# Kernel optimization log

Hardware: AMD Instinct MI355X
Metric: run time of the kernel (lower is better)

The kernel has to match this reference:

```python
import jax, jax.numpy as jnp
import numpy as np

N = 100_000      # nodes
E = 1_600_000    # edges
F_IN = 512       # input node features
H = 128          # hidden (num_hidden)
C = 64           # num_classes


def setup_inputs() -> dict:
    key = jax.random.key(0)
    ks = jax.random.split(key, 16)
    def lin(k, fi, fo):
        return (jax.random.normal(k, (fi, fo), jnp.float32) / np.sqrt(fi)).astype(jnp.float32)
    inp = {
        'x': jax.random.normal(ks[0], (N, F_IN), jnp.float32),
        'edge_index': jax.random.randint(ks[1], (2, E), 0, N, jnp.int32),
        'W0': lin(ks[2], F_IN, H), 'b0': jnp.zeros((H,), jnp.float32),
        'W1': lin(ks[3], H, H),    'b1': jnp.zeros((H,), jnp.float32),
        'W2': lin(ks[4], H, H),    'b2': jnp.zeros((H,), jnp.float32),
        'fc1_w': lin(ks[5], H, H), 'fc1_b': jnp.zeros((H,), jnp.float32),
        'fc2_w': lin(ks[6], H, H), 'fc2_b': jnp.zeros((H,), jnp.float32),
        'fc3_w': lin(ks[7], H, C), 'fc3_b': jnp.zeros((C,), jnp.float32),
    }
    return inp


def _gcn_norm(edge_index):
    # PyG GCNConv: add self-loops, symmetric normalization deg^-1/2 A deg^-1/2
    src = jnp.concatenate([edge_index[0], jnp.arange(N, dtype=edge_index.dtype)])
    dst = jnp.concatenate([edge_index[1], jnp.arange(N, dtype=edge_index.dtype)])
    deg = jax.ops.segment_sum(jnp.ones_like(dst, jnp.float32), dst, num_segments=N)
    dinv = jnp.where(deg > 0, jax.lax.rsqrt(deg), 0.0)
    norm = dinv[src] * dinv[dst]  # [E+N]
    return src, dst, norm


def _gcn_conv(x, W, b, src, dst, norm):
    h = x @ W + b                      # [N, H] transform first (fewer flops when F_in > H)
    msg = h[src] * norm[:, None]       # gather + scale, [E+N, H]
    return jax.ops.segment_sum(msg, dst, num_segments=N)  # scatter-add


def reference(x, edge_index, W0, b0, W1, b1, W2, b2,
              fc1_w, fc1_b, fc2_w, fc2_b, fc3_w, fc3_b):
    src, dst, norm = _gcn_norm(edge_index)
    y = jax.nn.relu(_gcn_conv(x, W0, b0, src, dst, norm))
    y = jax.nn.relu(_gcn_conv(y, W1, b1, src, dst, norm))
    y = jax.nn.relu(_gcn_conv(y, W2, b2, src, dst, norm))
    y = jax.nn.relu(y @ fc1_w + fc1_b)
    y = jax.nn.relu(y @ fc2_w + fc2_b)
    y = y @ fc3_w + fc3_b
    return jax.nn.log_softmax(y, axis=1)
```

## Files before the change

kernel.cpp:

```cpp
#include <hip/hip_runtime.h>
#include <hip/hip_bf16.h>
#include <cstdint>

typedef __hip_bfloat16 bf16;
typedef __hip_bfloat162 bf162;
typedef __bf16 bf16x8 __attribute__((ext_vector_type(8)));
typedef float f32x4 __attribute__((ext_vector_type(4)));

__global__ void detect_kernel(const unsigned short* __restrict__ xr, int* __restrict__ flag) {
  if (threadIdx.x == 0 && blockIdx.x == 0) {
    int pass = 0;
    for (int i = 0; i < 64; ++i) {
      unsigned short h = xr[2 * i];
      int e = (h >> 7) & 0xFF;
      if (e >= 110 && e <= 140) pass++;
    }
    *flag = (pass >= 32) ? 1 : 0;
  }
}

struct CvtDesc {
  const void* src;
  void* dst;
  int n, fi, fo, mode;
};
struct CvtAll { CvtDesc d[12]; };

__global__ void convert_all_kernel(CvtAll all, const int* __restrict__ flag) {
  CvtDesc dd = all.d[blockIdx.y];
  int isbf = *flag;
  for (int i = blockIdx.x * blockDim.x + threadIdx.x; i < dd.n; i += gridDim.x * blockDim.x) {
    float v = isbf ? __bfloat162float(((const bf16*)dd.src)[i]) : ((const float*)dd.src)[i];
    if (dd.mode) {
      int k = i / dd.fo, nn = i - k * dd.fo;
      ((__bf16*)dd.dst)[(size_t)nn * dd.fi + k] = (__bf16)v;
    } else {
      ((float*)dd.dst)[i] = v;
    }
  }
}


__global__ void count_kernel(const int* __restrict__ dst, int* __restrict__ deg, int E) {
  int i = blockIdx.x * blockDim.x + threadIdx.x;
  if (i < E) atomicAdd(&deg[dst[i]], 1);
}

__global__ void dinv_kernel(const int* __restrict__ deg, float* __restrict__ dinv, int n) {
  int i = blockIdx.x * blockDim.x + threadIdx.x;
  if (i < n) dinv[i] = rsqrtf((float)(deg[i] + 1));
}

__global__ void scan_block_kernel(const int* __restrict__ counts, int* __restrict__ excl,
                                  int* __restrict__ bsum, int n) {
  __shared__ int sd[1024];
  int t = threadIdx.x;
  int i = blockIdx.x * 1024 + t;
  int v = (i < n) ? counts[i] : 0;
  sd[t] = v;
  __syncthreads();
  for (int off = 1; off < 1024; off <<= 1) {
    int x = (t >= off) ? sd[t - off] : 0;
    __syncthreads();
    sd[t] += x;
    __syncthreads();
  }
  if (i < n) excl[i] = sd[t] - v;
  if (t == 1023) bsum[blockIdx.x] = sd[1023];
}

__global__ void scan_sums_kernel(int* __restrict__ bsum, int nb, int* __restrict__ row_ptr, int n) {
  __shared__ int sd[1024];
  int t = threadIdx.x;
  int v = (t < nb) ? bsum[t] : 0;
  sd[t] = v;
  __syncthreads();
  for (int off = 1; off < 1024; off <<= 1) {
    int x = (t >= off) ? sd[t - off] : 0;
    __syncthreads();
    sd[t] += x;
    __syncthreads();
  }
  if (t < nb) bsum[t] = sd[t] - v;
  if (t == 1023) row_ptr[n] = sd[1023];
}

__global__ void scan_add_kernel(int* __restrict__ excl, const int* __restrict__ bsum, int n) {
  int i = blockIdx.x * blockDim.x + threadIdx.x;
  if (i < n) excl[i] += bsum[i >> 10];
}

__global__ void fill_kernel(const int* __restrict__ src, const int* __restrict__ dst,
                            const int* __restrict__ row_ptr, int* __restrict__ cursor,
                            int* __restrict__ col, int E) {
  int i = blockIdx.x * blockDim.x + threadIdx.x;
  if (i < E) {
    int d = dst[i];
    int pos = row_ptr[d] + atomicAdd(&cursor[d], 1);
    col[pos] = src[i];
  }
}

__device__ __forceinline__ void gload_lds16(const void* g, void* l) {
  __builtin_amdgcn_global_load_lds(
      (const __attribute__((address_space(1))) void*)g,
      (__attribute__((address_space(3))) void*)l, 16, 0, 0);
}


template <int K, int ADUAL>
__global__ __launch_bounds__(256) void gemm_mfma_kernel(
    const void* __restrict__ Ain, const __bf16* __restrict__ Bt,
    const float* __restrict__ bias, bf16* __restrict__ C,
    int M, const float* __restrict__ rowscale, int do_relu,
    const int* __restrict__ flag) {
  constexpr int BK = 64;
  constexpr int NT = K / BK;
  __shared__ __align__(16) __bf16 As[2][128 * BK];
  __shared__ __align__(16) __bf16 Bs[2][128 * BK];

  const int abf = ADUAL ? flag[0] : 1;
  int t = threadIdx.x;
  int wave = t >> 6, lane = t & 63;
  int l15 = lane & 15, quad = lane >> 4;
  int wm = wave >> 1, wn = wave & 1;
  int rowbase = blockIdx.x * 128;
  const __bf16* Ab = (const __bf16*)Ain;
  const float* Af = (const float*)Ain;

  int srow = t >> 3;
  int sslot = t & 7;
  int xslot = sslot ^ (srow & 7);

  int sArow[4];
#pragma unroll
  for (int i = 0; i < 4; ++i) {
    int r = rowbase + i * 32 + srow;
    sArow[i] = (r < M) ? r : (M - 1);
  }

  f32x4 acc[4][4];
#pragma unroll
  for (int mt = 0; mt < 4; ++mt)
#pragma unroll
    for (int nt = 0; nt < 4; ++nt) acc[mt][nt] = (f32x4){0.f, 0.f, 0.f, 0.f};

  auto stage = [&](int kt, int buf) {
    int kbase = kt * BK + xslot * 8;
    if (abf) {
#pragma unroll
      for (int i = 0; i < 4; ++i)
        gload_lds16(Ab + (size_t)sArow[i] * K + kbase, &As[buf][t * 8 + i * 2048]);
    } else {
#pragma unroll
      for (int i = 0; i < 4; ++i) {
        const float* p = Af + (size_t)sArow[i] * K + kbase;
        bf16x8 v;
#pragma unroll
        for (int j = 0; j < 8; ++j) v[j] = (__bf16)p[j];
        *(bf16x8*)&As[buf][t * 8 + i * 2048] = v;
      }
    }
#pragma unroll
    for (int i = 0; i < 4; ++i)
      gload_lds16(Bt + (size_t)(i * 32 + srow) * K + kbase, &Bs[buf][t * 8 + i * 2048]);
  };

  auto compute = [&](int buf) {
#pragma unroll
    for (int c = 0; c < 2; ++c) {
      bf16x8 av[4], bv[4];
#pragma unroll
      for (int mt = 0; mt < 4; ++mt) {
        int row = wm * 64 + mt * 16 + l15;
        int slot = (c * 4 + quad) ^ (row & 7);
        av[mt] = *(const bf16x8*)&As[buf][row * BK + slot * 8];
      }
#pragma unroll
      for (int nt = 0; nt < 4; ++nt) {
        int row = wn * 64 + nt * 16 + l15;
        int slot = (c * 4 + quad) ^ (row & 7);
        bv[nt] = *(const bf16x8*)&Bs[buf][row * BK + slot * 8];
      }
#pragma unroll
      for (int mt = 0; mt < 4; ++mt)
#pragma unroll
        for (int nt = 0; nt < 4; ++nt)
          acc[mt][nt] =
              __builtin_amdgcn_mfma_f32_16x16x32_bf16(av[mt], bv[nt], acc[mt][nt], 0, 0, 0);
    }
  };

  stage(0, 0);
  __syncthreads();
#pragma unroll
  for (int kt = 0; kt < NT; ++kt) {
    int cur = kt & 1;
    if (kt + 1 < NT) stage(kt + 1, cur ^ 1);
    compute(cur);
    __syncthreads();
  }

#pragma unroll
  for (int mt = 0; mt < 4; ++mt) {
    int r0 = rowbase + wm * 64 + mt * 16 + quad * 4;
#pragma unroll
    for (int nt = 0; nt < 4; ++nt) {
      int c = wn * 64 + nt * 16 + l15;
      float bs = bias[c];
#pragma unroll
      for (int i = 0; i < 4; ++i) {
        int r = r0 + i;
        if (r < M) {
          float v = acc[mt][nt][i] + bs;
          if (rowscale) v *= rowscale[r];
          if (do_relu) v = fmaxf(v, 0.f);
          C[(size_t)r * 128 + c] = __float2bfloat16(v);
        }
      }
    }
  }
}


__global__ __launch_bounds__(256) void gather_kernel(
    const bf16* __restrict__ g, const int* __restrict__ row_ptr, const int* __restrict__ col,
    const float* __restrict__ dinv, bf16* __restrict__ y, int n) {
  int wave = threadIdx.x >> 6;
  int lane = threadIdx.x & 63;
  int node = blockIdx.x * 4 + wave;
  if (node >= n) return;
  const bf162* gp = (const bf162*)g;
  bf162 sv = gp[(size_t)node * 64 + lane];
  float ax = __bfloat162float(sv.x), ay = __bfloat162float(sv.y);
  float bx = 0.f, by = 0.f;
  int beg = row_ptr[node], end = row_ptr[node + 1];
  for (int e = beg; e < end; e += 8) {
    int s[8];
    float msk[8];
#pragma unroll
    for (int j = 0; j < 8; ++j) {
      int ee = e + j;
      bool ok = ee < end;
      s[j] = col[ok ? ee : e];
      msk[j] = ok ? 1.f : 0.f;
    }
    bf162 v[8];
#pragma unroll
    for (int j = 0; j < 8; ++j) v[j] = gp[(size_t)s[j] * 64 + lane];
#pragma unroll
    for (int j = 0; j < 8; j += 2) {
      ax = fmaf(msk[j], __bfloat162float(v[j].x), ax);
      ay = fmaf(msk[j], __bfloat162float(v[j].y), ay);
      bx = fmaf(msk[j + 1], __bfloat162float(v[j + 1].x), bx);
      by = fmaf(msk[j + 1], __bfloat162float(v[j + 1].y), by);
    }
  }
  float dv = dinv[node];
  float ox = fmaxf((ax + bx) * dv, 0.f);
  float oy = fmaxf((ay + by) * dv, 0.f);
  bf162 o;
  o.x = __float2bfloat16(ox);
  o.y = __float2bfloat16(oy);
  ((bf162*)y)[(size_t)node * 64 + lane] = o;
}


__global__ __launch_bounds__(256) void fc3_softmax_mfma_kernel(
    const bf16* __restrict__ y, const __bf16* __restrict__ Wt,
    const float* __restrict__ b, void* __restrict__ out, int M,
    const int* __restrict__ flag) {
  const int isbf = flag[0];
  int t = threadIdx.x;
  int wave = t >> 6, lane = t & 63;
  int l15 = lane & 15, quad = lane >> 4;
  int rowbase = blockIdx.x * 256 + wave * 64;

  f32x4 acc[4][4];
#pragma unroll
  for (int mt = 0; mt < 4; ++mt)
#pragma unroll
    for (int nt = 0; nt < 4; ++nt) acc[mt][nt] = (f32x4){0.f, 0.f, 0.f, 0.f};

  int arow[4];
#pragma unroll
  for (int mt = 0; mt < 4; ++mt) {
    int r = rowbase + mt * 16 + l15;
    arow[mt] = (r < M) ? r : (M - 1);
  }

  bf16x8 aA[4], bA[4], aB[4], bB[4];

  auto load_chunk = [&](int kc, bf16x8 (&av)[4], bf16x8 (&bv)[4]) {
    int ko = kc + quad * 8;
#pragma unroll
    for (int mt = 0; mt < 4; ++mt)
      av[mt] = *(const bf16x8*)(y + (size_t)arow[mt] * 128 + ko);
#pragma unroll
    for (int nt = 0; nt < 4; ++nt)
      bv[nt] = *(const bf16x8*)(Wt + (size_t)(nt * 16 + l15) * 128 + ko);
  };

  auto mfma16 = [&](const bf16x8 (&av)[4], const bf16x8 (&bv)[4]) {
#pragma unroll
    for (int mt = 0; mt < 4; ++mt)
#pragma unroll
      for (int nt = 0; nt < 4; ++nt)
        acc[mt][nt] =
            __builtin_amdgcn_mfma_f32_16x16x32_bf16(av[mt], bv[nt], acc[mt][nt], 0, 0, 0);
  };

  load_chunk(0, aA, bA);
  load_chunk(32, aB, bB);
  mfma16(aA, bA);
  load_chunk(64, aA, bA);
  mfma16(aB, bB);
  load_chunk(96, aB, bB);
  mfma16(aA, bA);
  mfma16(aB, bB);

  float bcol[4];
#pragma unroll
  for (int nt = 0; nt < 4; ++nt) bcol[nt] = b[nt * 16 + l15];

#pragma unroll
  for (int mt = 0; mt < 4; ++mt) {
#pragma unroll
    for (int i = 0; i < 4; ++i) {
      int r = rowbase + mt * 16 + quad * 4 + i;
      float v0 = acc[mt][0][i] + bcol[0];
      float v1 = acc[mt][1][i] + bcol[1];
      float v2 = acc[mt][2][i] + bcol[2];
      float v3 = acc[mt][3][i] + bcol[3];
      float m = fmaxf(fmaxf(v0, v1), fmaxf(v2, v3));
#pragma unroll
      for (int off = 8; off > 0; off >>= 1) m = fmaxf(m, __shfl_xor(m, off, 16));
      float s = __expf(v0 - m) + __expf(v1 - m) + __expf(v2 - m) + __expf(v3 - m);
#pragma unroll
      for (int off = 8; off > 0; off >>= 1) s += __shfl_xor(s, off, 16);
      float ls = m + __logf(s);
      if (r < M) {
        if (isbf) {
          bf16* op = (bf16*)out + (size_t)r * 64 + l15;
          op[0] = __float2bfloat16(v0 - ls);
          op[16] = __float2bfloat16(v1 - ls);
          op[32] = __float2bfloat16(v2 - ls);
          op[48] = __float2bfloat16(v3 - ls);
        } else {
          float* op = (float*)out + (size_t)r * 64 + l15;
          op[0] = v0 - ls;
          op[16] = v1 - ls;
          op[32] = v2 - ls;
          op[48] = v3 - ls;
        }
      }
    }
  }
}


extern "C" void kernel_launch(void* const* d_in, const int* in_sizes, int n_in,
                              void* d_out, int out_size, void* d_ws, size_t ws_size,
                              hipStream_t stream) {
  const void* x = d_in[0];
  const int* ei = (const int*)d_in[1];

  const int N = in_sizes[0] / 512;
  const int E = in_sizes[1] / 2;
  const int* srcp = ei;
  const int* dstp = ei + E;

  char* ws = (char*)d_ws;
  size_t off = 0;
  auto alloc = [&](size_t bytes) {
    void* p = ws + off;
    off = (off + bytes + 255) & ~(size_t)255;
    return p;
  };
  int*    flag    = (int*)alloc(4);
  int*    deg     = (int*)alloc((size_t)N * 4);
  int*    cursor  = (int*)alloc((size_t)N * 4);
  int*    row_ptr = (int*)alloc((size_t)(N + 1) * 4);
  int*    col     = (int*)alloc((size_t)E * 4);
  float*  dinv    = (float*)alloc((size_t)N * 4);
  int*    bsum    = (int*)alloc(1024 * 4);
  __bf16* W0t     = (__bf16*)alloc((size_t)512 * 128 * 2);
  __bf16* W1t     = (__bf16*)alloc((size_t)128 * 128 * 2);
  __bf16* W2t     = (__bf16*)alloc((size_t)128 * 128 * 2);
  __bf16* fc1t    = (__bf16*)alloc((size_t)128 * 128 * 2);
  __bf16* fc2t    = (__bf16*)alloc((size_t)128 * 128 * 2);
  __bf16* fc3t    = (__bf16*)alloc((size_t)64 * 128 * 2);
  float*  b0f     = (float*)alloc(128 * 4);
  float*  b1f     = (float*)alloc(128 * 4);
  float*  b2f     = (float*)alloc(128 * 4);
  float*  fc1bf   = (float*)alloc(128 * 4);
  float*  fc2bf   = (float*)alloc(128 * 4);
  float*  fc3bf   = (float*)alloc(64 * 4);
  bf16*   gbuf    = (bf16*)alloc((size_t)N * 128 * 2);
  bf16*   ybuf    = (bf16*)alloc((size_t)N * 128 * 2);

  const int tb = 256;

  detect_kernel<<<1, 64, 0, stream>>>((const unsigned short*)x, flag);

  CvtAll ca;
  ca.d[0]  = {d_in[2],  W0t,   512 * 128, 512, 128, 1};
  ca.d[1]  = {d_in[4],  W1t,   128 * 128, 128, 128, 1};
  ca.d[2]  = {d_in[6],  W2t,   128 * 128, 128, 128, 1};
  ca.d[3]  = {d_in[8],  fc1t,  128 * 128, 128, 128, 1};
  ca.d[4]  = {d_in[10], fc2t,  128 * 128, 128, 128, 1};
  ca.d[5]  = {d_in[3],  b0f,   128, 0, 0, 0};
  ca.d[6]  = {d_in[5],  b1f,   128, 0, 0, 0};
  ca.d[7]  = {d_in[7],  b2f,   128, 0, 0, 0};
  ca.d[8]  = {d_in[9],  fc1bf, 128, 0, 0, 0};
  ca.d[9]  = {d_in[11], fc2bf, 128, 0, 0, 0};
  ca.d[10] = {d_in[12], fc3t,  128 * 64, 128, 64, 1};
  ca.d[11] = {d_in[13], fc3bf, 64, 0, 0, 0};
  convert_all_kernel<<<dim3(64, 12), 256, 0, stream>>>(ca, flag);

  hipMemsetAsync(deg, 0, (size_t)N * 4, stream);
  hipMemsetAsync(cursor, 0, (size_t)N * 4, stream);

  count_kernel<<<(E + tb - 1) / tb, tb, 0, stream>>>(dstp, deg, E);
  dinv_kernel<<<(N + tb - 1) / tb, tb, 0, stream>>>(deg, dinv, N);
  int nb = (N + 1023) / 1024;
  scan_block_kernel<<<nb, 1024, 0, stream>>>(deg, row_ptr, bsum, N);
  scan_sums_kernel<<<1, 1024, 0, stream>>>(bsum, nb, row_ptr, N);
  scan_add_kernel<<<(N + tb - 1) / tb, tb, 0, stream>>>(row_ptr, bsum, N);
  fill_kernel<<<(E + tb - 1) / tb, tb, 0, stream>>>(srcp, dstp, row_ptr, cursor, col, E);

  int gemm_blocks = (N + 127) / 128;
  int gat_blocks = (N + 3) / 4;
  int fc3_blocks = (N + 255) / 256;

  gemm_mfma_kernel<512, 1><<<gemm_blocks, 256, 0, stream>>>(x, W0t, b0f, gbuf, N, dinv, 0, flag);
  gather_kernel<<<gat_blocks, 256, 0, stream>>>(gbuf, row_ptr, col, dinv, ybuf, N);
  gemm_mfma_kernel<128, 0><<<gemm_blocks, 256, 0, stream>>>(ybuf, W1t, b1f, gbuf, N, dinv, 0, flag);
  gather_kernel<<<gat_blocks, 256, 0, stream>>>(gbuf, row_ptr, col, dinv, ybuf, N);
  gemm_mfma_kernel<128, 0><<<gemm_blocks, 256, 0, stream>>>(ybuf, W2t, b2f, gbuf, N, dinv, 0, flag);
  gather_kernel<<<gat_blocks, 256, 0, stream>>>(gbuf, row_ptr, col, dinv, ybuf, N);
  gemm_mfma_kernel<128, 0><<<gemm_blocks, 256, 0, stream>>>(ybuf, fc1t, fc1bf, gbuf, N, nullptr, 1, flag);
  gemm_mfma_kernel<128, 0><<<gemm_blocks, 256, 0, stream>>>(gbuf, fc2t, fc2bf, ybuf, N, nullptr, 1, flag);
  fc3_softmax_mfma_kernel<<<fc3_blocks, 256, 0, stream>>>(ybuf, fc3t, fc3bf, d_out, N, flag);
}
```

Baseline: 828.2 us.

## Fuse fc1, fc2, fc3 and log-softmax into one kernel with LDS intermediates

Replaces the two separate 128x128 GEMM launches and the fc3+softmax kernel with a single kernel. Each block computes 128 rows through all three layers and keeps the intermediate activations in padded shared-memory tiles. This avoids two global round-trips of the N x 128 bf16 activations and two kernel launches. In exchange it uses about 68KB of LDS per block, which may lower occupancy, and adds block-wide syncs between the stages.

```diff
diff --git a/kernel.cpp b/kernel.cpp
--- a/kernel.cpp
+++ b/kernel.cpp
@@ -266,41 +266,31 @@
 }
 
 
-__global__ __launch_bounds__(256) void fc3_softmax_mfma_kernel(
-    const bf16* __restrict__ y, const __bf16* __restrict__ Wt,
-    const float* __restrict__ b, void* __restrict__ out, int M,
+__global__ __launch_bounds__(256) void fc_chain_kernel(
+    const bf16* __restrict__ yin, const __bf16* __restrict__ W1t,
+    const float* __restrict__ b1, const __bf16* __restrict__ W2t,
+    const float* __restrict__ b2, const __bf16* __restrict__ W3t,
+    const float* __restrict__ b3, void* __restrict__ out, int M,
     const int* __restrict__ flag) {
+  constexpr int LDH = 136;
+  __shared__ __align__(16) __bf16 h1[128 * LDH];
+  __shared__ __align__(16) __bf16 h2[128 * LDH];
   const int isbf = flag[0];
   int t = threadIdx.x;
   int wave = t >> 6, lane = t & 63;
   int l15 = lane & 15, quad = lane >> 4;
-  int rowbase = blockIdx.x * 256 + wave * 64;
+  int wm = wave >> 1, wn = wave & 1;
+  int rowbase = blockIdx.x * 128;
 
   f32x4 acc[4][4];
-#pragma unroll
-  for (int mt = 0; mt < 4; ++mt)
-#pragma unroll
-    for (int nt = 0; nt < 4; ++nt) acc[mt][nt] = (f32x4){0.f, 0.f, 0.f, 0.f};
-
-  int arow[4];
-#pragma unroll
-  for (int mt = 0; mt < 4; ++mt) {
-    int r = rowbase + mt * 16 + l15;
-    arow[mt] = (r < M) ? r : (M - 1);
-  }
-
   bf16x8 aA[4], bA[4], aB[4], bB[4];
 
-  auto load_chunk = [&](int kc, bf16x8 (&av)[4], bf16x8 (&bv)[4]) {
-    int ko = kc + quad * 8;
+  auto zacc = [&]() {
 #pragma unroll
     for (int mt = 0; mt < 4; ++mt)
-      av[mt] = *(const bf16x8*)(y + (size_t)arow[mt] * 128 + ko);
-#pragma unroll
-    for (int nt = 0; nt < 4; ++nt)
-      bv[nt] = *(const bf16x8*)(Wt + (size_t)(nt * 16 + l15) * 128 + ko);
-  };
-
+#pragma unroll
+      for (int nt = 0; nt < 4; ++nt) acc[mt][nt] = (f32x4){0.f, 0.f, 0.f, 0.f};
+  };
   auto mfma16 = [&](const bf16x8 (&av)[4], const bf16x8 (&bv)[4]) {
 #pragma unroll
     for (int mt = 0; mt < 4; ++mt)
@@ -310,28 +300,121 @@
             __builtin_amdgcn_mfma_f32_16x16x32_bf16(av[mt], bv[nt], acc[mt][nt], 0, 0, 0);
   };
 
-  load_chunk(0, aA, bA);
-  load_chunk(32, aB, bB);
+  int arow[4];
+#pragma unroll
+  for (int mt = 0; mt < 4; ++mt) {
+    int r = rowbase + wm * 64 + mt * 16 + l15;
+    arow[mt] = (r < M) ? r : (M - 1);
+  }
+  auto ld1 = [&](int kc, bf16x8 (&av)[4], bf16x8 (&bv)[4]) {
+    int ko = kc + quad * 8;
+#pragma unroll
+    for (int mt = 0; mt < 4; ++mt)
+      av[mt] = *(const bf16x8*)(yin + (size_t)arow[mt] * 128 + ko);
+#pragma unroll
+    for (int nt = 0; nt < 4; ++nt)
+      bv[nt] = *(const bf16x8*)(W1t + (size_t)(wn * 64 + nt * 16 + l15) * 128 + ko);
+  };
+  zacc();
+  ld1(0, aA, bA);
+  ld1(32, aB, bB);
   mfma16(aA, bA);
-  load_chunk(64, aA, bA);
+  ld1(64, aA, bA);
   mfma16(aB, bB);
-  load_chunk(96, aB, bB);
+  ld1(96, aB, bB);
   mfma16(aA, bA);
   mfma16(aB, bB);
+#pragma unroll
+  for (int mt = 0; mt < 4; ++mt) {
+    int rl0 = wm * 64 + mt * 16 + quad * 4;
+#pragma unroll
+    for (int nt = 0; nt < 4; ++nt) {
+      int c = wn * 64 + nt * 16 + l15;
+      float bs = b1[c];
+#pragma unroll
+      for (int i = 0; i < 4; ++i)
+        h1[(rl0 + i) * LDH + c] = (__bf16)fmaxf(acc[mt][nt][i] + bs, 0.f);
+    }
+  }
+  __syncthreads();
+
+  auto ld2 = [&](int kc, bf16x8 (&av)[4], bf16x8 (&bv)[4]) {
+    int ko = kc + quad * 8;
+#pragma unroll
+    for (int mt = 0; mt < 4; ++mt)
+      av[mt] = *(const bf16x8*)&h1[(wm * 64 + mt * 16 + l15) * LDH + ko];
+#pragma unroll
+    for (int nt = 0; nt < 4; ++nt)
+      bv[nt] = *(const bf16x8*)(W2t + (size_t)(wn * 64 + nt * 16 + l15) * 128 + ko);
+  };
+  zacc();
+  ld2(0, aA, bA);
+  ld2(32, aB, bB);
+  mfma16(aA, bA);
+  ld2(64, aA, bA);
+  mfma16(aB, bB);
+  ld2(96, aB, bB);
+  mfma16(aA, bA);
+  mfma16(aB, bB);
+#pragma unroll
+  for (int mt = 0; mt < 4; ++mt) {
+    int rl0 = wm * 64 + mt * 16 + quad * 4;
+#pragma unroll
+    for (int nt = 0; nt < 4; ++nt) {
+      int c = wn * 64 + nt * 16 + l15;
+      float bs = b2[c];
+#pragma unroll
+      for (int i = 0; i < 4; ++i)
+        h2[(rl0 + i) * LDH + c] = (__bf16)fmaxf(acc[mt][nt][i] + bs, 0.f);
+    }
+  }
+  __syncthreads();
+
+  f32x4 acc3[2][4];
+#pragma unroll
+  for (int mt = 0; mt < 2; ++mt)
+#pragma unroll
+    for (int nt = 0; nt < 4; ++nt) acc3[mt][nt] = (f32x4){0.f, 0.f, 0.f, 0.f};
+  bf16x8 a3A[2], a3B[2];
+  auto ld3 = [&](int kc, bf16x8 (&av)[2], bf16x8 (&bv)[4]) {
+    int ko = kc + quad * 8;
+#pragma unroll
+    for (int mt = 0; mt < 2; ++mt)
+      av[mt] = *(const bf16x8*)&h2[(wave * 32 + mt * 16 + l15) * LDH + ko];
+#pragma unroll
+    for (int nt = 0; nt < 4; ++nt)
+      bv[nt] = *(const bf16x8*)(W3t + (size_t)(nt * 16 + l15) * 128 + ko);
+  };
+  auto mfma8 = [&](const bf16x8 (&av)[2], const bf16x8 (&bv)[4]) {
+#pragma unroll
+    for (int mt = 0; mt < 2; ++mt)
+#pragma unroll
+      for (int nt = 0; nt < 4; ++nt)
+        acc3[mt][nt] =
+            __builtin_amdgcn_mfma_f32_16x16x32_bf16(av[mt], bv[nt], acc3[mt][nt], 0, 0, 0);
+  };
+  ld3(0, a3A, bA);
+  ld3(32, a3B, bB);
+  mfma8(a3A, bA);
+  ld3(64, a3A, bA);
+  mfma8(a3B, bB);
+  ld3(96, a3B, bB);
+  mfma8(a3A, bA);
+  mfma8(a3B, bB);
 
   float bcol[4];
 #pragma unroll
-  for (int nt = 0; nt < 4; ++nt) bcol[nt] = b[nt * 16 + l15];
-
-#pragma unroll
-  for (int mt = 0; mt < 4; ++mt) {
+  for (int nt = 0; nt < 4; ++nt) bcol[nt] = b3[nt * 16 + l15];
+
+#pragma unroll
+  for (int mt = 0; mt < 2; ++mt) {
 #pragma unroll
     for (int i = 0; i < 4; ++i) {
-      int r = rowbase + mt * 16 + quad * 4 + i;
-      float v0 = acc[mt][0][i] + bcol[0];
-      float v1 = acc[mt][1][i] + bcol[1];
-      float v2 = acc[mt][2][i] + bcol[2];
-      float v3 = acc[mt][3][i] + bcol[3];
+      int r = rowbase + wave * 32 + mt * 16 + quad * 4 + i;
+      float v0 = acc3[mt][0][i] + bcol[0];
+      float v1 = acc3[mt][1][i] + bcol[1];
+      float v2 = acc3[mt][2][i] + bcol[2];
+      float v3 = acc3[mt][3][i] + bcol[3];
       float m = fmaxf(fmaxf(v0, v1), fmaxf(v2, v3));
 #pragma unroll
       for (int off = 8; off > 0; off >>= 1) m = fmaxf(m, __shfl_xor(m, off, 16));
@@ -431,7 +514,6 @@
 
   int gemm_blocks = (N + 127) / 128;
   int gat_blocks = (N + 3) / 4;
-  int fc3_blocks = (N + 255) / 256;
 
   gemm_mfma_kernel<512, 1><<<gemm_blocks, 256, 0, stream>>>(x, W0t, b0f, gbuf, N, dinv, 0, flag);
   gather_kernel<<<gat_blocks, 256, 0, stream>>>(gbuf, row_ptr, col, dinv, ybuf, N);
@@ -439,7 +521,6 @@
   gather_kernel<<<gat_blocks, 256, 0, stream>>>(gbuf, row_ptr, col, dinv, ybuf, N);
   gemm_mfma_kernel<128, 0><<<gemm_blocks, 256, 0, stream>>>(ybuf, W2t, b2f, gbuf, N, dinv, 0, flag);
   gather_kernel<<<gat_blocks, 256, 0, stream>>>(gbuf, row_ptr, col, dinv, ybuf, N);
-  gemm_mfma_kernel<128, 0><<<gemm_blocks, 256, 0, stream>>>(ybuf, fc1t, fc1bf, gbuf, N, nullptr, 1, flag);
-  gemm_mfma_kernel<128, 0><<<gemm_blocks, 256, 0, stream>>>(gbuf, fc2t, fc2bf, ybuf, N, nullptr, 1, flag);
-  fc3_softmax_mfma_kernel<<<fc3_blocks, 256, 0, stream>>>(ybuf, fc3t, fc3bf, d_out, N, flag);
-}
+  fc_chain_kernel<<<gemm_blocks, 256, 0, stream>>>(ybuf, fc1t, fc1bf, fc2t, fc2bf,
+                                                   fc3t, fc3bf, d_out, N, flag);
+}
```

Result: faster. 808.4 us (-2.4%).
